# Kernel tuning notes

Measured on AMD Instinct MI355X. Metric: run time of the kernel, lower is better.

Reference implementation:

```python
import jax, jax.numpy as jnp
import numpy as np

N_EMBD = 1024
N_HEAD = 16
B, T = 2, 2048

def setup_inputs() -> dict:
    key = jax.random.key(0)
    ks = jax.random.split(key, 5)
    s = 1.0 / np.sqrt(N_EMBD)
    return {
        'x': jax.random.normal(ks[0], (B, T, N_EMBD), jnp.float32),
        'W_attn': jax.random.normal(ks[1], (N_EMBD, 3 * N_EMBD), jnp.float32) * s,
        'b_attn': jax.random.normal(ks[2], (3 * N_EMBD,), jnp.float32) * 0.02,
        'W_proj': jax.random.normal(ks[3], (N_EMBD, N_EMBD), jnp.float32) * s,
        'b_proj': jax.random.normal(ks[4], (N_EMBD,), jnp.float32) * 0.02,
    }

def reference(x, W_attn, b_attn, W_proj, b_proj):
    Bx, Tx, C = x.shape
    H = N_HEAD
    D = C // H  # head dim
    qkv = x @ W_attn + b_attn                      # [B,T,3C]
    q, k, v = jnp.split(qkv, 3, axis=-1)
    # [B,T,C] -> [B,H,T,D]
    q = q.reshape(Bx, Tx, H, D).transpose(0, 2, 1, 3)
    k = k.reshape(Bx, Tx, H, D).transpose(0, 2, 1, 3)
    v = v.reshape(Bx, Tx, H, D).transpose(0, 2, 1, 3)
    scale = 1.0 / jnp.sqrt(jnp.asarray(D, x.dtype))
    scores = jnp.einsum('bhqd,bhkd->bhqk', q, k) * scale   # [B,H,T,T]
    causal = jnp.tril(jnp.ones((Tx, Tx), bool))
    scores = jnp.where(causal, scores, jnp.asarray(-jnp.inf, scores.dtype))
    attn = jax.nn.softmax(scores, axis=-1)
    y = jnp.einsum('bhqk,bhkd->bhqd', attn, v)              # [B,H,T,D]
    y = y.transpose(0, 2, 1, 3).reshape(Bx, Tx, C)
    return y @ W_proj + b_proj
```

## Files before the change

kernel.cpp:

```cpp
#include <hip/hip_runtime.h>
#include <stdint.h>

typedef float f32x4 __attribute__((ext_vector_type(4)));
typedef float f32x16 __attribute__((ext_vector_type(16)));
typedef __bf16 bf16x8 __attribute__((ext_vector_type(8)));
typedef unsigned short ushort8 __attribute__((ext_vector_type(8)));
typedef unsigned int uint4v __attribute__((ext_vector_type(4)));
typedef unsigned short u16;

#define DEVINL static __device__ __forceinline__

#define EXP2(x) exp2f(x)

#define VMCNT(N)                                          \
  {                                                       \
    asm volatile("s_waitcnt vmcnt(" #N ")" ::: "memory"); \
    __builtin_amdgcn_sched_barrier(0);                    \
  }

DEVINL void barrier_raw() {
  __builtin_amdgcn_sched_barrier(0);
  __builtin_amdgcn_s_barrier();
  __builtin_amdgcn_sched_barrier(0);
}

DEVINL u16 f2bf(float f) {
  __bf16 h = (__bf16)f;
  return __builtin_bit_cast(u16, h);
}

DEVINL unsigned cvtpk(float lo, float hi) {
  unsigned r;
  asm("v_cvt_pk_bf16_f32 %0, %1, %2" : "=v"(r) : "v"(lo), "v"(hi));
  return r;
}

DEVINL void plswap(unsigned& a, unsigned& b) {
  asm("v_permlane32_swap_b32 %0, %1" : "+v"(a), "+v"(b));
}

DEVINL void gload16(const void* g, void* l) {
  __builtin_amdgcn_global_load_lds((__attribute__((address_space(1))) void*)g,
                                   (__attribute__((address_space(3))) void*)l, 16, 0, 0);
}

DEVINL f32x4 mfma16(bf16x8 a, bf16x8 b, f32x4 c) {
  return __builtin_amdgcn_mfma_f32_16x16x32_bf16(a, b, c, 0, 0, 0);
}
DEVINL f32x16 mfma32(bf16x8 a, bf16x8 b, f32x16 c) {
  return __builtin_amdgcn_mfma_f32_32x32x16_bf16(a, b, c, 0, 0, 0);
}

__global__ __launch_bounds__(256) void k_cast_bf16(const float* __restrict__ in,
                                                   u16* __restrict__ out) {
  const int i = blockIdx.x * 256 + threadIdx.x;
  const float4* p = (const float4*)in + (size_t)i * 2;
  float4 a = p[0], b = p[1];
  ushort8 o;
  o[0] = f2bf(a.x); o[1] = f2bf(a.y); o[2] = f2bf(a.z); o[3] = f2bf(a.w);
  o[4] = f2bf(b.x); o[5] = f2bf(b.y); o[6] = f2bf(b.z); o[7] = f2bf(b.w);
  *((ushort8*)out + i) = o;
}

__global__ __launch_bounds__(256) void k_tcast(const float* __restrict__ in,
                                               u16* __restrict__ out, int R, int C) {
  __shared__ float tile[32][33];
  const int tx = threadIdx.x & 31, ty = threadIdx.x >> 5;
  const int c0 = blockIdx.x * 32, r0 = blockIdx.y * 32;
#pragma unroll
  for (int k = 0; k < 4; ++k)
    tile[ty + k * 8][tx] = in[(size_t)(r0 + ty + k * 8) * C + (c0 + tx)];
  __syncthreads();
#pragma unroll
  for (int k = 0; k < 4; ++k)
    out[(size_t)(c0 + ty + k * 8) * R + (r0 + tx)] = f2bf(tile[tx][ty + k * 8]);
}

DEVINL void stage128x64(const u16* __restrict__ g, int ld, u16* lds, int t) {
#pragma unroll
  for (int i = 0; i < 4; ++i) {
    int ci = i * 256 + t;
    int row = ci >> 3, gr = ci & 7;
    int gs = gr ^ (row & 7);
    gload16(g + (size_t)row * ld + gs * 8, lds + ci * 8);
  }
}

DEVINL void gemm_core(const u16* __restrict__ A, const u16* __restrict__ B, int Kdim,
                      u16* As, u16* Bs, int t, f32x4 acc[4][4]) {
  const int l = t & 63, lr = l & 15, lg = l >> 4;
  const int wr = t >> 7, wc = (t >> 6) & 1;
  const int nk = Kdim >> 6;
  stage128x64(A, Kdim, As, t);
  stage128x64(B, Kdim, Bs, t);
  for (int kt = 0; kt < nk; ++kt) {
    if (kt + 1 < nk) {
      const int nx = ((kt + 1) & 1) * 8192;
      stage128x64(A + (kt + 1) * 64, Kdim, As + nx, t);
      stage128x64(B + (kt + 1) * 64, Kdim, Bs + nx, t);
      VMCNT(8);
    } else {
      VMCNT(0);
    }
    barrier_raw();
    const u16* Asc = As + (kt & 1) * 8192;
    const u16* Bsc = Bs + (kt & 1) * 8192;
#pragma unroll
    for (int ks = 0; ks < 2; ++ks) {
      bf16x8 af[4], bf[4];
#pragma unroll
      for (int mi = 0; mi < 4; ++mi) {
        int r = wr * 64 + mi * 16 + lr;
        int g = (ks * 4 + lg) ^ (r & 7);
        af[mi] = *(const bf16x8*)(Asc + r * 64 + g * 8);
      }
#pragma unroll
      for (int ni = 0; ni < 4; ++ni) {
        int r = wc * 64 + ni * 16 + lr;
        int g = (ks * 4 + lg) ^ (r & 7);
        bf[ni] = *(const bf16x8*)(Bsc + r * 64 + g * 8);
      }
#pragma unroll
      for (int mi = 0; mi < 4; ++mi)
#pragma unroll
        for (int ni = 0; ni < 4; ++ni)
          acc[mi][ni] = mfma16(af[mi], bf[ni], acc[mi][ni]);
    }
    barrier_raw();
  }
}

__global__ __launch_bounds__(256) void k_gemm_qkv(const u16* __restrict__ xb,
                                                  const u16* __restrict__ WaT,
                                                  const float* __restrict__ b_attn,
                                                  u16* __restrict__ Qo,
                                                  u16* __restrict__ Ko,
                                                  u16* __restrict__ Vto) {
  __shared__ u16 As[2 * 128 * 64], Bs[2 * 128 * 64];
  const int t = threadIdx.x;
  const int m0 = blockIdx.y * 128, n0 = blockIdx.x * 128;
  f32x4 acc[4][4] = {};
  gemm_core(xb + (size_t)m0 * 1024, WaT + (size_t)n0 * 1024, 1024, As, Bs, t, acc);
  const int l = t & 63, lr = l & 15, lg = l >> 4;
  const int wr = t >> 7, wc = (t >> 6) & 1;
#pragma unroll
  for (int ni = 0; ni < 4; ++ni) {
    const int gcol = n0 + wc * 64 + ni * 16 + lr;
    const int part = gcol >> 10;
    const int h = (gcol & 1023) >> 6, d = gcol & 63;
    const float bias = b_attn[gcol];
    if (part == 2) {
#pragma unroll
      for (int mi = 0; mi < 4; ++mi) {
        const int tt0 = m0 + wr * 64 + mi * 16 + lg * 4;
        const int bb = tt0 >> 11, tt = tt0 & 2047;
        ushort4 pk;
        pk.x = f2bf(acc[mi][ni][0] + bias);
        pk.y = f2bf(acc[mi][ni][1] + bias);
        pk.z = f2bf(acc[mi][ni][2] + bias);
        pk.w = f2bf(acc[mi][ni][3] + bias);
        *(ushort4*)(Vto + (size_t)(bb * 16 + h) * 131072 + (size_t)d * 2048 + tt) = pk;
      }
    } else {
      const float osc = (part == 0) ? 0.18033688f : 1.0f;
      u16* dst = (part == 0) ? Qo : Ko;
#pragma unroll
      for (int mi = 0; mi < 4; ++mi)
#pragma unroll
        for (int r = 0; r < 4; ++r) {
          const int grow = m0 + wr * 64 + mi * 16 + lg * 4 + r;
          const int bb = grow >> 11, tt = grow & 2047;
          dst[(size_t)((bb * 16 + h) * 2048 + tt) * 64 + d] =
              f2bf((acc[mi][ni][r] + bias) * osc);
        }
    }
  }
}

__global__ __launch_bounds__(256) void k_gemm_proj(const u16* __restrict__ Yb,
                                                   const u16* __restrict__ WpT,
                                                   const float* __restrict__ b_proj,
                                                   float* __restrict__ out) {
  __shared__ u16 As[2 * 128 * 64], Bs[2 * 128 * 64];
  const int t = threadIdx.x;
  const int m0 = blockIdx.y * 128, n0 = blockIdx.x * 128;
  f32x4 acc[4][4] = {};
  gemm_core(Yb + (size_t)m0 * 1024, WpT + (size_t)n0 * 1024, 1024, As, Bs, t, acc);
  const int l = t & 63, lr = l & 15, lg = l >> 4;
  const int wr = t >> 7, wc = (t >> 6) & 1;
#pragma unroll
  for (int ni = 0; ni < 4; ++ni) {
    const int gcol = n0 + wc * 64 + ni * 16 + lr;
    const float bias = b_proj[gcol];
#pragma unroll
    for (int mi = 0; mi < 4; ++mi)
#pragma unroll
      for (int r = 0; r < 4; ++r) {
        const int grow = m0 + wr * 64 + mi * 16 + lg * 4 + r;
        out[(size_t)grow * 1024 + gcol] = acc[mi][ni][r] + bias;
      }
  }
}

__global__ __launch_bounds__(512, 4) void k_flash(const u16* __restrict__ Q,
                                                  const u16* __restrict__ K,
                                                  const u16* __restrict__ Vt,
                                                  u16* __restrict__ Y) {
  __shared__ u16 Ks[2][4096];
  __shared__ u16 Vs[2][4096];
  __shared__ float Ms[4][64][33];
  const int t = threadIdx.x, l = t & 63, w = t >> 6;
  const int ql = l & 31, hi = l >> 5;
  const int wq = w & 3, wk = w >> 2;
  const int bid = blockIdx.x;
  const int u = bid >> 3;
  const int qt = 15 - (u >> 2);
  const int bh = (bid & 7) + 8 * (u & 3);
  const size_t base = (size_t)bh * 131072;
  const int b = bh >> 4, hh = bh & 15;
  const int qbase = qt * 128 + wq * 32;
  const int qrow = qbase + ql;
  const int nkt = 2 * qt + 2;

  bf16x8 qb[4];
#pragma unroll
  for (int m = 0; m < 4; ++m)
    qb[m] = *(const bf16x8*)(Q + base + (size_t)qrow * 64 + hi * 8 + 16 * m);

  {
    int row = t >> 3, g = t & 7, gs = g ^ (row & 7);
    gload16(K + base + (size_t)row * 64 + gs * 8, Ks[0] + t * 8);
    gload16(Vt + base + (size_t)row * 2048 + gs * 8, Vs[0] + t * 8);
  }

  f32x16 accO0 = {}, accO1 = {};
  float rs_lane = 0.f;
  const int krow = wk * 32 + ql;
  const int kswz = krow & 7;

#define STEP(CUR, KT)                                                                 \
  {                                                                                   \
    if ((KT) + 1 < nkt) {                                                             \
      int row = t >> 3, g = t & 7, gs = g ^ (row & 7);                                \
      gload16(K + base + (size_t)(((KT) + 1) * 64 + row) * 64 + gs * 8,               \
              Ks[CUR ^ 1] + t * 8);                                                   \
      gload16(Vt + base + (size_t)row * 2048 + ((KT) + 1) * 64 + gs * 8,              \
              Vs[CUR ^ 1] + t * 8);                                                   \
      VMCNT(2);                                                                       \
    } else {                                                                          \
      VMCNT(0);                                                                       \
    }                                                                                 \
    barrier_raw();                               \
    const int kbase = (KT) * 64 + wk * 32;                                            \
    if (kbase <= qbase + 31) {                   \
      f32x16 st = {};                                                                 \
      __builtin_amdgcn_s_setprio(1);                                                  \
      _Pragma("unroll") for (int m = 0; m < 4; ++m) {                                 \
        bf16x8 ka = *(const bf16x8*)(Ks[CUR] + krow * 64 + (((hi + 2 * m) ^ kswz) * 8)); \
        st = mfma32(ka, qb[m], st);                                                   \
      }                                                                               \
      __builtin_amdgcn_s_setprio(0);                                                  \
      if (kbase + 31 > qbase) {                            \
        _Pragma("unroll") for (int r = 0; r < 16; ++r) {                              \
          const int keyl = (r & 3) + 8 * (r >> 2) + 4 * hi;                           \
          if (kbase + keyl > qrow) st[r] = -1e30f;                                    \
        }                                                                             \
      }                                                                               \
      float p[16];                                                                    \
      _Pragma("unroll") for (int r = 0; r < 16; ++r) {                                \
        p[r] = EXP2(st[r]);                                                           \
        rs_lane += p[r];                                                              \
      }                                                                               \
      unsigned uu[8];                                                                 \
      _Pragma("unroll") for (int i = 0; i < 8; ++i) uu[i] = cvtpk(p[2 * i], p[2 * i + 1]); \
      plswap(uu[0], uu[2]);                                                           \
      plswap(uu[1], uu[3]);                                                           \
      plswap(uu[4], uu[6]);                                                           \
      plswap(uu[5], uu[7]);                                                           \
      uint4v w0 = {uu[0], uu[1], uu[2], uu[3]};                                       \
      uint4v w1 = {uu[4], uu[5], uu[6], uu[7]};                                       \
      bf16x8 pf0 = __builtin_bit_cast(bf16x8, w0);                                    \
      bf16x8 pf1 = __builtin_bit_cast(bf16x8, w1);                                    \
      __builtin_amdgcn_s_setprio(1);                                                  \
      {                                                                               \
        const int vr0 = ql, vz0 = vr0 & 7;                                            \
        bf16x8 va0 = *(const bf16x8*)(Vs[CUR] + vr0 * 64 + (((wk * 4 + hi) ^ vz0) * 8)); \
        bf16x8 va1 =                                                                  \
            *(const bf16x8*)(Vs[CUR] + vr0 * 64 + (((wk * 4 + 2 + hi) ^ vz0) * 8));   \
        accO0 = mfma32(va0, pf0, accO0);                                              \
        accO0 = mfma32(va1, pf1, accO0);                                              \
        const int vr1 = 32 + ql, vz1 = vr1 & 7;                                       \
        bf16x8 vb0 = *(const bf16x8*)(Vs[CUR] + vr1 * 64 + (((wk * 4 + hi) ^ vz1) * 8)); \
        bf16x8 vb1 =                                                                  \
            *(const bf16x8*)(Vs[CUR] + vr1 * 64 + (((wk * 4 + 2 + hi) ^ vz1) * 8));   \
        accO1 = mfma32(vb0, pf0, accO1);                                              \
        accO1 = mfma32(vb1, pf1, accO1);                                              \
      }                                                                               \
      __builtin_amdgcn_s_setprio(0);                                                  \
    }                                                                                 \
    barrier_raw();                                   \
  }

  for (int kt = 0; kt < nkt; kt += 2) {
    STEP(0, kt);
    STEP(1, kt + 1);
  }
#undef STEP

  rs_lane += __shfl_xor(rs_lane, 32);

  if (wk == 1) {
    float* Mp = &Ms[wq][l][0];
#pragma unroll
    for (int i = 0; i < 16; ++i) Mp[i] = accO0[i];
#pragma unroll
    for (int i = 0; i < 16; ++i) Mp[16 + i] = accO1[i];
    Mp[32] = rs_lane;
  }
  __syncthreads();
  if (wk == 0) {
    const float* Mp = &Ms[wq][l][0];
    const float inv = 1.0f / (rs_lane + Mp[32]);
    u16* yb = Y + ((size_t)(b * 2048 + qrow)) * 1024 + hh * 64;
#pragma unroll
    for (int rq = 0; rq < 4; ++rq) {
      const int d0 = 8 * rq + 4 * hi;
      ushort4 o4;
      o4.x = f2bf((accO0[rq * 4 + 0] + Mp[rq * 4 + 0]) * inv);
      o4.y = f2bf((accO0[rq * 4 + 1] + Mp[rq * 4 + 1]) * inv);
      o4.z = f2bf((accO0[rq * 4 + 2] + Mp[rq * 4 + 2]) * inv);
      o4.w = f2bf((accO0[rq * 4 + 3] + Mp[rq * 4 + 3]) * inv);
      *(ushort4*)(yb + d0) = o4;
    }
#pragma unroll
    for (int rq = 0; rq < 4; ++rq) {
      const int d0 = 32 + 8 * rq + 4 * hi;
      ushort4 o4;
      o4.x = f2bf((accO1[rq * 4 + 0] + Mp[16 + rq * 4 + 0]) * inv);
      o4.y = f2bf((accO1[rq * 4 + 1] + Mp[16 + rq * 4 + 1]) * inv);
      o4.z = f2bf((accO1[rq * 4 + 2] + Mp[16 + rq * 4 + 2]) * inv);
      o4.w = f2bf((accO1[rq * 4 + 3] + Mp[16 + rq * 4 + 3]) * inv);
      *(ushort4*)(yb + d0) = o4;
    }
  }
}

extern "C" void kernel_launch(void* const* d_in, const int* in_sizes, int n_in,
                              void* d_out, int out_size, void* d_ws, size_t ws_size,
                              hipStream_t stream) {
  const float* x      = (const float*)d_in[0];
  const float* W_attn = (const float*)d_in[1];
  const float* b_attn = (const float*)d_in[2];
  const float* W_proj = (const float*)d_in[3];
  const float* b_proj = (const float*)d_in[4];
  float* out = (float*)d_out;

  char* ws = (char*)d_ws;
  u16* xb  = (u16*)(ws);
  u16* WaT = (u16*)(ws + (8u  << 20));
  u16* WpT = (u16*)(ws + (14u << 20));
  u16* Qb  = (u16*)(ws + (16u << 20));
  u16* Kb  = (u16*)(ws + (24u << 20));
  u16* Vtb = (u16*)(ws + (32u << 20));
  u16* Yb  = (u16*)(ws + (40u << 20));

  k_cast_bf16<<<dim3(2048), dim3(256), 0, stream>>>(x, xb);
  k_tcast<<<dim3(96, 32), dim3(256), 0, stream>>>(W_attn, WaT, 1024, 3072);
  k_tcast<<<dim3(32, 32), dim3(256), 0, stream>>>(W_proj, WpT, 1024, 1024);
  k_gemm_qkv<<<dim3(24, 32), dim3(256), 0, stream>>>(xb, WaT, b_attn, Qb, Kb, Vtb);
  k_flash<<<dim3(512), dim3(512), 0, stream>>>(Qb, Kb, Vtb, Yb);
  k_gemm_proj<<<dim3(8, 32), dim3(256), 0, stream>>>(Yb, WpT, b_proj, out);
}
```

Before: 121.9 us.

## Restructure flash kernel: 1024-thread blocks, paired causal q-tiles, 128-key steps

The flash attention kernel now launches 256 blocks of 1024 threads. Each block processes two q-tiles, p and 15-p, so the causal work per block is balanced. Each step covers 128 keys split across 4 key-warp groups, and the partial outputs are combined with a two-stage tree reduction in shared memory. Global-to-LDS async loads with an XOR swizzle are replaced by register-staged loads written to padded LDS rows. This cuts the step count and removes tail imbalance, at the cost of extra syncs, the reduction work and a less latency-hiding prefetch.

```diff
diff --git a/kernel.cpp b/kernel.cpp
--- a/kernel.cpp
+++ b/kernel.cpp
@@ -202,145 +202,171 @@
   }
 }
 
-__global__ __launch_bounds__(512, 4) void k_flash(const u16* __restrict__ Q,
-                                                  const u16* __restrict__ K,
-                                                  const u16* __restrict__ Vt,
-                                                  u16* __restrict__ Y) {
-  __shared__ u16 Ks[2][4096];
-  __shared__ u16 Vs[2][4096];
-  __shared__ float Ms[4][64][33];
+__global__ __launch_bounds__(1024, 4) void k_flash(const u16* __restrict__ Q,
+                                                   const u16* __restrict__ K,
+                                                   const u16* __restrict__ Vt,
+                                                   u16* __restrict__ Y) {
+  __shared__ u16 SM[2 * 9216 + 2 * 8704];
+  u16* KsB = SM;
+  u16* VsB = SM + 2 * 9216;
+  float* Ms = (float*)SM;
+
   const int t = threadIdx.x, l = t & 63, w = t >> 6;
   const int ql = l & 31, hi = l >> 5;
   const int wq = w & 3, wk = w >> 2;
   const int bid = blockIdx.x;
-  const int u = bid >> 3;
-  const int qt = 15 - (u >> 2);
-  const int bh = (bid & 7) + 8 * (u & 3);
+  const int bh = (bid & 7) + 8 * ((bid >> 3) & 3);
+  const int p = bid >> 5;
   const size_t base = (size_t)bh * 131072;
   const int b = bh >> 4, hh = bh & 15;
-  const int qbase = qt * 128 + wq * 32;
-  const int qrow = qbase + ql;
-  const int nkt = 2 * qt + 2;
-
-  bf16x8 qb[4];
-#pragma unroll
-  for (int m = 0; m < 4; ++m)
-    qb[m] = *(const bf16x8*)(Q + base + (size_t)qrow * 64 + hi * 8 + 16 * m);
-
-  {
-    int row = t >> 3, g = t & 7, gs = g ^ (row & 7);
-    gload16(K + base + (size_t)row * 64 + gs * 8, Ks[0] + t * 8);
-    gload16(Vt + base + (size_t)row * 2048 + gs * 8, Vs[0] + t * 8);
-  }
-
-  f32x16 accO0 = {}, accO1 = {};
-  float rs_lane = 0.f;
-  const int krow = wk * 32 + ql;
-  const int kswz = krow & 7;
-
-#define STEP(CUR, KT)                                                                 \
-  {                                                                                   \
-    if ((KT) + 1 < nkt) {                                                             \
-      int row = t >> 3, g = t & 7, gs = g ^ (row & 7);                                \
-      gload16(K + base + (size_t)(((KT) + 1) * 64 + row) * 64 + gs * 8,               \
-              Ks[CUR ^ 1] + t * 8);                                                   \
-      gload16(Vt + base + (size_t)row * 2048 + ((KT) + 1) * 64 + gs * 8,              \
-              Vs[CUR ^ 1] + t * 8);                                                   \
-      VMCNT(2);                                                                       \
-    } else {                                                                          \
-      VMCNT(0);                                                                       \
-    }                                                                                 \
-    barrier_raw();                               \
-    const int kbase = (KT) * 64 + wk * 32;                                            \
-    if (kbase <= qbase + 31) {                   \
-      f32x16 st = {};                                                                 \
-      __builtin_amdgcn_s_setprio(1);                                                  \
-      _Pragma("unroll") for (int m = 0; m < 4; ++m) {                                 \
-        bf16x8 ka = *(const bf16x8*)(Ks[CUR] + krow * 64 + (((hi + 2 * m) ^ kswz) * 8)); \
-        st = mfma32(ka, qb[m], st);                                                   \
-      }                                                                               \
-      __builtin_amdgcn_s_setprio(0);                                                  \
-      if (kbase + 31 > qbase) {                            \
-        _Pragma("unroll") for (int r = 0; r < 16; ++r) {                              \
-          const int keyl = (r & 3) + 8 * (r >> 2) + 4 * hi;                           \
-          if (kbase + keyl > qrow) st[r] = -1e30f;                                    \
-        }                                                                             \
-      }                                                                               \
-      float p[16];                                                                    \
-      _Pragma("unroll") for (int r = 0; r < 16; ++r) {                                \
-        p[r] = EXP2(st[r]);                                                           \
-        rs_lane += p[r];                                                              \
-      }                                                                               \
-      unsigned uu[8];                                                                 \
-      _Pragma("unroll") for (int i = 0; i < 8; ++i) uu[i] = cvtpk(p[2 * i], p[2 * i + 1]); \
-      plswap(uu[0], uu[2]);                                                           \
-      plswap(uu[1], uu[3]);                                                           \
-      plswap(uu[4], uu[6]);                                                           \
-      plswap(uu[5], uu[7]);                                                           \
-      uint4v w0 = {uu[0], uu[1], uu[2], uu[3]};                                       \
-      uint4v w1 = {uu[4], uu[5], uu[6], uu[7]};                                       \
-      bf16x8 pf0 = __builtin_bit_cast(bf16x8, w0);                                    \
-      bf16x8 pf1 = __builtin_bit_cast(bf16x8, w1);                                    \
-      __builtin_amdgcn_s_setprio(1);                                                  \
-      {                                                                               \
-        const int vr0 = ql, vz0 = vr0 & 7;                                            \
-        bf16x8 va0 = *(const bf16x8*)(Vs[CUR] + vr0 * 64 + (((wk * 4 + hi) ^ vz0) * 8)); \
-        bf16x8 va1 =                                                                  \
-            *(const bf16x8*)(Vs[CUR] + vr0 * 64 + (((wk * 4 + 2 + hi) ^ vz0) * 8));   \
-        accO0 = mfma32(va0, pf0, accO0);                                              \
-        accO0 = mfma32(va1, pf1, accO0);                                              \
-        const int vr1 = 32 + ql, vz1 = vr1 & 7;                                       \
-        bf16x8 vb0 = *(const bf16x8*)(Vs[CUR] + vr1 * 64 + (((wk * 4 + hi) ^ vz1) * 8)); \
-        bf16x8 vb1 =                                                                  \
-            *(const bf16x8*)(Vs[CUR] + vr1 * 64 + (((wk * 4 + 2 + hi) ^ vz1) * 8));   \
-        accO1 = mfma32(vb0, pf0, accO1);                                              \
-        accO1 = mfma32(vb1, pf1, accO1);                                              \
-      }                                                                               \
-      __builtin_amdgcn_s_setprio(0);                                                  \
-    }                                                                                 \
-    barrier_raw();                                   \
-  }
-
-  for (int kt = 0; kt < nkt; kt += 2) {
-    STEP(0, kt);
-    STEP(1, kt + 1);
-  }
-#undef STEP
-
-  rs_lane += __shfl_xor(rs_lane, 32);
-
-  if (wk == 1) {
-    float* Mp = &Ms[wq][l][0];
-#pragma unroll
-    for (int i = 0; i < 16; ++i) Mp[i] = accO0[i];
-#pragma unroll
-    for (int i = 0; i < 16; ++i) Mp[16 + i] = accO1[i];
-    Mp[32] = rs_lane;
-  }
-  __syncthreads();
-  if (wk == 0) {
-    const float* Mp = &Ms[wq][l][0];
-    const float inv = 1.0f / (rs_lane + Mp[32]);
-    u16* yb = Y + ((size_t)(b * 2048 + qrow)) * 1024 + hh * 64;
-#pragma unroll
-    for (int rq = 0; rq < 4; ++rq) {
-      const int d0 = 8 * rq + 4 * hi;
-      ushort4 o4;
-      o4.x = f2bf((accO0[rq * 4 + 0] + Mp[rq * 4 + 0]) * inv);
-      o4.y = f2bf((accO0[rq * 4 + 1] + Mp[rq * 4 + 1]) * inv);
-      o4.z = f2bf((accO0[rq * 4 + 2] + Mp[rq * 4 + 2]) * inv);
-      o4.w = f2bf((accO0[rq * 4 + 3] + Mp[rq * 4 + 3]) * inv);
-      *(ushort4*)(yb + d0) = o4;
-    }
-#pragma unroll
-    for (int rq = 0; rq < 4; ++rq) {
-      const int d0 = 32 + 8 * rq + 4 * hi;
-      ushort4 o4;
-      o4.x = f2bf((accO1[rq * 4 + 0] + Mp[16 + rq * 4 + 0]) * inv);
-      o4.y = f2bf((accO1[rq * 4 + 1] + Mp[16 + rq * 4 + 1]) * inv);
-      o4.z = f2bf((accO1[rq * 4 + 2] + Mp[16 + rq * 4 + 2]) * inv);
-      o4.w = f2bf((accO1[rq * 4 + 3] + Mp[16 + rq * 4 + 3]) * inv);
-      *(ushort4*)(yb + d0) = o4;
+  const int srow = t >> 3, scol = t & 7;
+  const int sd = t >> 4, sck = t & 15;
+
+  for (int half = 0; half < 2; ++half) {
+    const int qt = half ? 15 - p : p;
+    const int nsteps = qt + 1;
+    const int qbase = qt * 128 + wq * 32;
+    const int qrow = qbase + ql;
+
+    __syncthreads();
+
+    bf16x8 qb[4];
+#pragma unroll
+    for (int m = 0; m < 4; ++m)
+      qb[m] = *(const bf16x8*)(Q + base + (size_t)qrow * 64 + hi * 8 + 16 * m);
+
+    {
+      ushort8 kv = *(const ushort8*)(K + base + (size_t)srow * 64 + scol * 8);
+      ushort8 vv = *(const ushort8*)(Vt + base + (size_t)sd * 2048 + sck * 8);
+      *(ushort8*)(KsB + srow * 72 + scol * 8) = kv;
+      *(ushort8*)(VsB + sd * 136 + sck * 8) = vv;
+    }
+    __syncthreads();
+
+    f32x16 accO0 = {}, accO1 = {};
+    float rs_lane = 0.f;
+    const int krow = wk * 32 + ql;
+
+    for (int n = 0; n < nsteps; ++n) {
+      const u16* Kc = KsB + (n & 1) * 9216;
+      const u16* Vc = VsB + (n & 1) * 8704;
+      const bool more = (n + 1 < nsteps);
+      ushort8 kv, vv;
+      if (more) {
+        kv = *(const ushort8*)(K + base + (size_t)((n + 1) * 128 + srow) * 64 + scol * 8);
+        vv = *(const ushort8*)(Vt + base + (size_t)sd * 2048 + (n + 1) * 128 + sck * 8);
+      }
+      const int kbase = n * 128 + wk * 32;
+      if (kbase <= qbase + 31) {
+        f32x16 st = {};
+        __builtin_amdgcn_s_setprio(1);
+#pragma unroll
+        for (int m = 0; m < 4; ++m) {
+          bf16x8 ka = *(const bf16x8*)(Kc + krow * 72 + (hi + 2 * m) * 8);
+          st = mfma32(ka, qb[m], st);
+        }
+        __builtin_amdgcn_s_setprio(0);
+        if (kbase + 31 > qbase) {
+#pragma unroll
+          for (int r = 0; r < 16; ++r) {
+            const int keyl = (r & 3) + 8 * (r >> 2) + 4 * hi;
+            if (kbase + keyl > qrow) st[r] = -1e30f;
+          }
+        }
+        float pp[16];
+#pragma unroll
+        for (int r = 0; r < 16; ++r) {
+          pp[r] = EXP2(st[r]);
+          rs_lane += pp[r];
+        }
+        unsigned uu[8];
+#pragma unroll
+        for (int i = 0; i < 8; ++i) uu[i] = cvtpk(pp[2 * i], pp[2 * i + 1]);
+        plswap(uu[0], uu[2]);
+        plswap(uu[1], uu[3]);
+        plswap(uu[4], uu[6]);
+        plswap(uu[5], uu[7]);
+        uint4v w0 = {uu[0], uu[1], uu[2], uu[3]};
+        uint4v w1 = {uu[4], uu[5], uu[6], uu[7]};
+        bf16x8 pf0 = __builtin_bit_cast(bf16x8, w0);
+        bf16x8 pf1 = __builtin_bit_cast(bf16x8, w1);
+        __builtin_amdgcn_s_setprio(1);
+        {
+          bf16x8 va0 = *(const bf16x8*)(Vc + ql * 136 + (4 * wk + hi) * 8);
+          bf16x8 va1 = *(const bf16x8*)(Vc + ql * 136 + (4 * wk + 2 + hi) * 8);
+          accO0 = mfma32(va0, pf0, accO0);
+          accO0 = mfma32(va1, pf1, accO0);
+          bf16x8 vb0 = *(const bf16x8*)(Vc + (32 + ql) * 136 + (4 * wk + hi) * 8);
+          bf16x8 vb1 = *(const bf16x8*)(Vc + (32 + ql) * 136 + (4 * wk + 2 + hi) * 8);
+          accO1 = mfma32(vb0, pf0, accO1);
+          accO1 = mfma32(vb1, pf1, accO1);
+        }
+        __builtin_amdgcn_s_setprio(0);
+      }
+      if (more) {
+        u16* Kn = KsB + ((n + 1) & 1) * 9216;
+        u16* Vn = VsB + ((n + 1) & 1) * 8704;
+        *(ushort8*)(Kn + srow * 72 + scol * 8) = kv;
+        *(ushort8*)(Vn + sd * 136 + sck * 8) = vv;
+      }
+      __syncthreads();
+    }
+
+    rs_lane += __shfl_xor(rs_lane, 32);
+
+    {
+      float* Mp = Ms + (size_t)(((wq * 2 + (wk >> 1)) * 64 + l)) * 33;
+      if (wk & 1) {
+#pragma unroll
+        for (int i = 0; i < 16; ++i) Mp[i] = accO0[i];
+#pragma unroll
+        for (int i = 0; i < 16; ++i) Mp[16 + i] = accO1[i];
+        Mp[32] = rs_lane;
+      }
+      __syncthreads();
+      if (!(wk & 1)) {
+#pragma unroll
+        for (int i = 0; i < 16; ++i) accO0[i] += Mp[i];
+#pragma unroll
+        for (int i = 0; i < 16; ++i) accO1[i] += Mp[16 + i];
+        rs_lane += Mp[32];
+      }
+      __syncthreads();
+    }
+    {
+      float* Mp = Ms + (size_t)((wq * 64 + l)) * 33;
+      if (wk == 2) {
+#pragma unroll
+        for (int i = 0; i < 16; ++i) Mp[i] = accO0[i];
+#pragma unroll
+        for (int i = 0; i < 16; ++i) Mp[16 + i] = accO1[i];
+        Mp[32] = rs_lane;
+      }
+      __syncthreads();
+      if (wk == 0) {
+        const float inv = 1.0f / (rs_lane + Mp[32]);
+        u16* yb = Y + ((size_t)(b * 2048 + qrow)) * 1024 + hh * 64;
+#pragma unroll
+        for (int rq = 0; rq < 4; ++rq) {
+          const int d0 = 8 * rq + 4 * hi;
+          ushort4 o4;
+          o4.x = f2bf((accO0[rq * 4 + 0] + Mp[rq * 4 + 0]) * inv);
+          o4.y = f2bf((accO0[rq * 4 + 1] + Mp[rq * 4 + 1]) * inv);
+          o4.z = f2bf((accO0[rq * 4 + 2] + Mp[rq * 4 + 2]) * inv);
+          o4.w = f2bf((accO0[rq * 4 + 3] + Mp[rq * 4 + 3]) * inv);
+          *(ushort4*)(yb + d0) = o4;
+        }
+#pragma unroll
+        for (int rq = 0; rq < 4; ++rq) {
+          const int d0 = 32 + 8 * rq + 4 * hi;
+          ushort4 o4;
+          o4.x = f2bf((accO1[rq * 4 + 0] + Mp[16 + rq * 4 + 0]) * inv);
+          o4.y = f2bf((accO1[rq * 4 + 1] + Mp[16 + rq * 4 + 1]) * inv);
+          o4.z = f2bf((accO1[rq * 4 + 2] + Mp[16 + rq * 4 + 2]) * inv);
+          o4.w = f2bf((accO1[rq * 4 + 3] + Mp[16 + rq * 4 + 3]) * inv);
+          *(ushort4*)(yb + d0) = o4;
+        }
+      }
     }
   }
 }
@@ -368,6 +394,6 @@
   k_tcast<<<dim3(96, 32), dim3(256), 0, stream>>>(W_attn, WaT, 1024, 3072);
   k_tcast<<<dim3(32, 32), dim3(256), 0, stream>>>(W_proj, WpT, 1024, 1024);
   k_gemm_qkv<<<dim3(24, 32), dim3(256), 0, stream>>>(xb, WaT, b_attn, Qb, Kb, Vtb);
-  k_flash<<<dim3(512), dim3(512), 0, stream>>>(Qb, Kb, Vtb, Yb);
+  k_flash<<<dim3(256), dim3(1024), 0, stream>>>(Qb, Kb, Vtb, Yb);
   k_gemm_proj<<<dim3(8, 32), dim3(256), 0, stream>>>(Yb, WpT, b_proj, out);
 }
```

Result: faster. 115.6 us (-5.1%).
